# Performance work log

Hardware: AMD Instinct MI355X
Metric: run time of the kernel (lower is better)

The kernel has to match this reference:

```python
import jax, jax.numpy as jnp
import numpy as np

N_NODES = 50000

def cheb_conv(x, edge_index, W, b):
    # PyG ChebConv, K=2, normalization='sym', lambda_max=2.0 (default):
    # scaled Laplacian L_hat = (2/lambda_max)*L - I = -D^{-1/2} A D^{-1/2} (zero diag).
    # Tx_0 = x, Tx_1 = L_hat @ x ; out = Tx_0 @ W[0] + Tx_1 @ W[1] + b
    src, dst = edge_index[0], edge_index[1]
    ones = jnp.ones(src.shape[0], x.dtype)
    deg = jax.ops.segment_sum(ones, src, num_segments=N_NODES)
    dinv = jnp.where(deg > 0, 1.0 / jnp.sqrt(deg), 0.0)
    norm = -dinv[src] * dinv[dst]                                   # [E]
    tx1 = jax.ops.segment_sum(x[src] * norm[:, None], dst, num_segments=N_NODES)
    return x @ W[0] + tx1 @ W[1] + b

def setup_inputs() -> dict:
    key = jax.random.key(0)
    ks = jax.random.split(key, 12)
    IN, OUT, E, P = 128, 2, 800000, 400000
    return {
        "x": jax.random.normal(ks[0], (N_NODES, IN), jnp.float32),
        "edge_index": jax.random.randint(ks[1], (2, E), 0, N_NODES),
        "E_pos": jax.random.randint(ks[2], (2, P), 0, N_NODES),
        "neg_edge_index": jax.random.randint(ks[3], (2, P), 0, N_NODES),
        "W1": jax.random.normal(ks[4], (2, IN, 300), jnp.float32) * 0.05,
        "b1": jnp.zeros((300,), jnp.float32),
        "W2": jax.random.normal(ks[5], (2, 300, 100), jnp.float32) * 0.05,
        "b2": jnp.zeros((100,), jnp.float32),
        "W3": jax.random.normal(ks[6], (2, 100, OUT), jnp.float32) * 0.05,
        "b3": jnp.zeros((OUT,), jnp.float32),
        "lin1_W": jax.random.normal(ks[7], (100, IN), jnp.float32) * 0.05,
        "lin1_b": jnp.zeros((100,), jnp.float32),
        "lin2_W": jax.random.normal(ks[8], (100, IN), jnp.float32) * 0.05,
        "lin2_b": jnp.zeros((100,), jnp.float32),
        "c1": jnp.full((1,), 0.5, jnp.float32),
        "c2": jnp.full((1,), 0.5, jnp.float32),
    }

def reference(x, edge_index, E_pos, neg_edge_index, W1, b1, W2, b2, W3, b3,
              lin1_W, lin1_b, lin2_W, lin2_b, c1, c2):
    # eval mode: F.dropout and dropout_edge are identity
    x0 = x
    h = jax.nn.relu(cheb_conv(x0, edge_index, W1, b1))
    x1 = jax.nn.relu(cheb_conv(h, edge_index, W2, b2))
    x2 = x1 + jax.nn.relu(x0 @ lin1_W.T + lin1_b)
    z = x1 + jax.nn.relu(x0 @ lin2_W.T + lin2_b)
    pos_score = jnp.sum(z[E_pos[0]] * z[E_pos[1]], axis=1)              # [P]
    pos_loss = -jnp.mean(jnp.log(jax.nn.sigmoid(pos_score) + 1e-15))
    neg_score = jnp.sum(z[neg_edge_index[0]] * z[neg_edge_index[1]], axis=1)
    neg_loss = -jnp.mean(jnp.log(1.0 - jax.nn.sigmoid(neg_score) + 1e-15))
    r_loss = pos_loss + neg_loss
    out = cheb_conv(x2, edge_index, W3, b3)                             # [N, out_channels]
    return (out, r_loss, c1, c2)
```

## Files before the change

### kernel.cpp

```cpp
#include <hip/hip_runtime.h>
#include <math.h>


typedef unsigned short ushort_t;
typedef unsigned char u8;
typedef __attribute__((ext_vector_type(8))) __bf16 bf16x8;
typedef __attribute__((ext_vector_type(8))) short s16x8;
typedef __attribute__((ext_vector_type(4))) float f32x4;
typedef __attribute__((ext_vector_type(2))) float f32x2;

__device__ __forceinline__ f32x4 mfma16x16x32(s16x8 a, s16x8 b, f32x4 c) {
  return __builtin_amdgcn_mfma_f32_16x16x32_bf16(
      __builtin_bit_cast(bf16x8, a), __builtin_bit_cast(bf16x8, b), c, 0, 0, 0);
}
__device__ __forceinline__ ushort_t f2bf(float f) {
  union { float f; unsigned u; } c; c.f = f;
  unsigned r = (c.u + 0x7FFFu + ((c.u >> 16) & 1u)) >> 16;
  return (ushort_t)r;
}
__device__ __forceinline__ float blo(unsigned u) {
  union { unsigned u; float f; } c; c.u = u << 16; return c.f;
}
__device__ __forceinline__ float bhi(unsigned u) {
  union { unsigned u; float f; } c; c.u = u & 0xffff0000u; return c.f;
}
__device__ __forceinline__ f32x2 cvt2lo(unsigned u) {
  return __builtin_amdgcn_cvt_pk_f32_fp8((int)u, false);
}
__device__ __forceinline__ f32x2 cvt2hi(unsigned u) {
  return __builtin_amdgcn_cvt_pk_f32_fp8((int)u, true);
}
__device__ __forceinline__ u8 f2fp8(float f) {
  return (u8)(__builtin_amdgcn_cvt_pk_fp8_f32(f, 0.f, 0, false) & 0xff);
}

template<int VAR, int NT, int KTOT>
__global__ __launch_bounds__(256) void gemm_mfma(
    const ushort_t* __restrict__ A0, const ushort_t* __restrict__ A1,
    const ushort_t* __restrict__ Wt,
    const float* __restrict__ bias0, const float* __restrict__ bias1,
    const float* __restrict__ x1,
    const float* __restrict__ W3c, const float* __restrict__ b3c,
    void* __restrict__ out0, void* __restrict__ out1,
    float* __restrict__ t0g, float* __restrict__ t1g, int M)
{
  constexpr int NF = NT / 32;
  __shared__ __align__(16) ushort_t As[64 * 40];
  __shared__ __align__(16) ushort_t Bs[NT * 40];
  __shared__ float w3s[400];
  const int tid  = threadIdx.x;
  const int lane = tid & 63, w = tid >> 6;
  const int m0 = blockIdx.x * 64;
  const int wm = (w & 1) * 32, wn = (w >> 1) * (NT / 2);
  if (VAR == 2) { for (int i = tid; i < 400; i += 256) w3s[i] = W3c[i]; }
  f32x4 acc[2][NF];
#pragma unroll
  for (int i = 0; i < 2; ++i)
#pragma unroll
    for (int j = 0; j < NF; ++j) acc[i][j] = (f32x4){0.f, 0.f, 0.f, 0.f};

  for (int k0 = 0; k0 < KTOT; k0 += 32) {
    {
      const int r = tid >> 2, c8 = (tid & 3) * 8;
      const int gm = m0 + r;
      uint4 v = {0u, 0u, 0u, 0u};
      if (gm < M) {
        const ushort_t* srcp;
        if (VAR == 0) srcp = (k0 < 128) ? A0 + (size_t)gm * 128 + k0 + c8
                                        : A1 + (size_t)gm * 128 + (k0 - 128) + c8;
        else if (VAR == 1) srcp = A0 + (size_t)gm * 320 + k0 + c8;
        else srcp = A0 + (size_t)gm * 128 + k0 + c8;
        v = *(const uint4*)srcp;
      }
      *(uint4*)&As[r * 40 + c8] = v;
    }
    {
      const int c8 = (tid & 3) * 8;
#pragma unroll
      for (int i = 0; i < (NT * 4 + 255) / 256; ++i) {
        const int r = (tid >> 2) + i * 64;
        if (r < NT)
          *(uint4*)&Bs[r * 40 + c8] = *(const uint4*)(Wt + (size_t)r * KTOT + k0 + c8);
      }
    }
    __syncthreads();
    s16x8 af[2], bfr[NF];
#pragma unroll
    for (int mi = 0; mi < 2; ++mi)
      af[mi] = *(const s16x8*)&As[(wm + mi * 16 + (lane & 15)) * 40 + (lane >> 4) * 8];
#pragma unroll
    for (int ni = 0; ni < NF; ++ni)
      bfr[ni] = *(const s16x8*)&Bs[(wn + ni * 16 + (lane & 15)) * 40 + (lane >> 4) * 8];
#pragma unroll
    for (int mi = 0; mi < 2; ++mi)
#pragma unroll
      for (int ni = 0; ni < NF; ++ni)
        acc[mi][ni] = mfma16x16x32(af[mi], bfr[ni], acc[mi][ni]);
    __syncthreads();
  }

  if (VAR == 2) {
#pragma unroll
    for (int mi = 0; mi < 2; ++mi)
#pragma unroll
      for (int r = 0; r < 4; ++r) {
        const int gRow = m0 + wm + mi * 16 + ((lane >> 4) << 2) + r;
        float p0 = 0.f, p1 = 0.f, p2 = 0.f, p3 = 0.f;
#pragma unroll
        for (int ni = 0; ni < NF; ++ni) {
          const int col = wn + ni * 16 + (lane & 15);
          const float v = acc[mi][ni][r];
          if (gRow < M) {
            if (col < 100) {
              const float x2v = x1[(size_t)gRow * 128 + col] + fmaxf(v + bias0[col], 0.f);
              p0 = fmaf(x2v, w3s[col * 2 + 0], p0);
              p1 = fmaf(x2v, w3s[col * 2 + 1], p1);
              p2 = fmaf(x2v, w3s[200 + col * 2 + 0], p2);
              p3 = fmaf(x2v, w3s[200 + col * 2 + 1], p3);
            } else if (col < 200) {
              const int c = col - 100;
              ((u8*)out1)[(size_t)gRow * 128 + c] =
                  f2fp8(x1[(size_t)gRow * 128 + c] + fmaxf(v + bias1[c], 0.f));
            }
          }
        }
        if (wn == 0) {
#pragma unroll
          for (int off = 8; off; off >>= 1) {
            p0 += __shfl_down(p0, off, 16);
            p1 += __shfl_down(p1, off, 16);
            p2 += __shfl_down(p2, off, 16);
            p3 += __shfl_down(p3, off, 16);
          }
          if ((lane & 15) == 0 && gRow < M) {
            t0g[(size_t)gRow * 2 + 0] = p0 + b3c[0];
            t0g[(size_t)gRow * 2 + 1] = p1 + b3c[1];
            t1g[(size_t)gRow * 2 + 0] = p2;
            t1g[(size_t)gRow * 2 + 1] = p3;
          }
        }
      }
  } else {
#pragma unroll
    for (int mi = 0; mi < 2; ++mi)
#pragma unroll
      for (int ni = 0; ni < NF; ++ni)
#pragma unroll
        for (int r = 0; r < 4; ++r) {
          const int gRow = m0 + wm + mi * 16 + ((lane >> 4) << 2) + r;
          const int col  = wn + ni * 16 + (lane & 15);
          if (gRow >= M) continue;
          const float v = acc[mi][ni][r];
          if (VAR == 0) {
            ushort_t* h = (ushort_t*)out0;
            h[(size_t)gRow * 320 + col] = (col < 300) ? f2bf(fmaxf(v + bias0[col], 0.f))
                                                      : (ushort_t)0;
          } else {
            if (col < 100) ((float*)out0)[(size_t)gRow * 128 + col] = v + bias0[col];
            else if (col < 200) ((u8*)out1)[(size_t)gRow * 128 + (col - 100)] = f2fp8(v);
          }
        }
  }
}

__global__ void cvt_x_kernel(const float* __restrict__ x, ushort_t* __restrict__ xb,
                             u8* __restrict__ xf8, int n4) {
  const int i = blockIdx.x * 256 + threadIdx.x;
  if (i < n4) {
    const float4 v = ((const float4*)x)[i];
    ushort4 o; o.x = f2bf(v.x); o.y = f2bf(v.y); o.z = f2bf(v.z); o.w = f2bf(v.w);
    ((ushort4*)xb)[i] = o;
    int p = 0;
    p = __builtin_amdgcn_cvt_pk_fp8_f32(v.x, v.y, p, false);
    p = __builtin_amdgcn_cvt_pk_fp8_f32(v.z, v.w, p, true);
    ((unsigned*)xf8)[i] = (unsigned)p;
  }
}
__global__ void pack_all(const float* __restrict__ W1, const float* __restrict__ W2,
                         const float* __restrict__ l1W, const float* __restrict__ l2W,
                         ushort_t* __restrict__ W1t, ushort_t* __restrict__ W2t,
                         ushort_t* __restrict__ Wlt) {
  const int i = blockIdx.x * 256 + threadIdx.x;
  if (i < 81920) {
    const int n = i >> 8, k = i & 255;
    float v = 0.f;
    if (n < 300) v = (k < 128) ? W1[k * 300 + n] : W1[38400 + (k - 128) * 300 + n];
    W1t[i] = f2bf(v);
  } else if (i < 153600) {
    const int j = i - 81920;
    const int n = j / 320, k = j - n * 320;
    float v = 0.f;
    if (n < 200 && k < 300) v = W2[(n < 100 ? 0 : 30000) + k * 100 + (n % 100)];
    W2t[j] = f2bf(v);
  } else if (i < 182272) {
    const int j = i - 153600;
    const int n = j >> 7, k = j & 127;
    float v = 0.f;
    if (n < 100) v = l1W[n * 128 + k];
    else if (n < 200) v = l2W[(n - 100) * 128 + k];
    Wlt[j] = f2bf(v);
  }
}

__global__ void deg_count_kernel(const int* __restrict__ src, const int* __restrict__ dst,
                                 float* __restrict__ deg, int* __restrict__ cnt, int E)
{
  const int e = blockIdx.x * blockDim.x + threadIdx.x;
  if (e < E) { atomicAdd(deg + src[e], 1.0f); atomicAdd(cnt + dst[e], 1); }
}
__global__ void dinv_kernel(float* __restrict__ d, int n) {
  const int i = blockIdx.x * blockDim.x + threadIdx.x;
  if (i < n) { const float v = d[i]; d[i] = (v > 0.f) ? 1.f / sqrtf(v) : 0.f; }
}

__global__ void scan_local(const int* __restrict__ cnt, int* __restrict__ ptr,
                           int* __restrict__ bsum, int n)
{
  __shared__ int tmp[256];
  const int i = blockIdx.x * 256 + threadIdx.x;
  const int v = (i < n) ? cnt[i] : 0;
  tmp[threadIdx.x] = v;
  __syncthreads();
  for (int off = 1; off < 256; off <<= 1) {
    const int t = (threadIdx.x >= off) ? tmp[threadIdx.x - off] : 0;
    __syncthreads();
    tmp[threadIdx.x] += t;
    __syncthreads();
  }
  if (i < n) ptr[i] = tmp[threadIdx.x] - v;
  if (threadIdx.x == 255) bsum[blockIdx.x] = tmp[255];
}
__global__ void scan_bsum(int* __restrict__ bsum, int nb) {
  __shared__ int tmp[256];
  const int v = (threadIdx.x < nb) ? bsum[threadIdx.x] : 0;
  tmp[threadIdx.x] = v;
  __syncthreads();
  for (int off = 1; off < 256; off <<= 1) {
    const int t = (threadIdx.x >= off) ? tmp[threadIdx.x - off] : 0;
    __syncthreads();
    tmp[threadIdx.x] += t;
    __syncthreads();
  }
  if (threadIdx.x < nb) bsum[threadIdx.x] = tmp[threadIdx.x] - v;
}
__global__ void scan_add(int* __restrict__ ptr, const int* __restrict__ bsum, int n, int E) {
  const int i = blockIdx.x * 256 + threadIdx.x;
  if (i < n) ptr[i] += bsum[blockIdx.x];
  if (i == 0) ptr[n] = E;
}
__global__ void fill_csr(const int* __restrict__ src, const int* __restrict__ dst,
                         const float* __restrict__ dinv, int* __restrict__ cur,
                         int* __restrict__ cs, float* __restrict__ cw, int E)
{
  const int e = blockIdx.x * blockDim.x + threadIdx.x;
  if (e >= E) return;
  const int s = src[e], d = dst[e];
  const int pos = atomicAdd(cur + d, 1);
  cs[pos] = s;
  cw[pos] = -dinv[s] * dinv[d];
}

#define ACCV(u, ww) { f32x2 t; \
  t = cvt2lo(u.x); a[0]  = fmaf(ww, t.x, a[0]);  a[1]  = fmaf(ww, t.y, a[1]);  \
  t = cvt2hi(u.x); a[2]  = fmaf(ww, t.x, a[2]);  a[3]  = fmaf(ww, t.y, a[3]);  \
  t = cvt2lo(u.y); a[4]  = fmaf(ww, t.x, a[4]);  a[5]  = fmaf(ww, t.y, a[5]);  \
  t = cvt2hi(u.y); a[6]  = fmaf(ww, t.x, a[6]);  a[7]  = fmaf(ww, t.y, a[7]);  \
  t = cvt2lo(u.z); a[8]  = fmaf(ww, t.x, a[8]);  a[9]  = fmaf(ww, t.y, a[9]);  \
  t = cvt2hi(u.z); a[10] = fmaf(ww, t.x, a[10]); a[11] = fmaf(ww, t.y, a[11]); \
  t = cvt2lo(u.w); a[12] = fmaf(ww, t.x, a[12]); a[13] = fmaf(ww, t.y, a[13]); \
  t = cvt2hi(u.w); a[14] = fmaf(ww, t.x, a[14]); a[15] = fmaf(ww, t.y, a[15]); }

__global__ __launch_bounds__(256) void gather128e(
    const u8* __restrict__ xf8, ushort_t* __restrict__ txb,
    const int* __restrict__ ptr, const int* __restrict__ cs,
    const float* __restrict__ cw, int M)
{
  const int node = (blockIdx.x * 256 + threadIdx.x) >> 3;
  const int sub  = threadIdx.x & 7;
  if (node >= M) return;
  const int beg = ptr[node], end = ptr[node + 1];
  float a[16] = {};
  int p = beg;
  for (; p + 4 <= end; p += 4) {
    const int s0 = cs[p], s1 = cs[p + 1], s2 = cs[p + 2], s3 = cs[p + 3];
    const float w0 = cw[p], w1 = cw[p + 1], w2 = cw[p + 2], w3 = cw[p + 3];
    const uint4 v0 = *(const uint4*)(xf8 + (size_t)s0 * 128 + sub * 16);
    const uint4 v1 = *(const uint4*)(xf8 + (size_t)s1 * 128 + sub * 16);
    const uint4 v2 = *(const uint4*)(xf8 + (size_t)s2 * 128 + sub * 16);
    const uint4 v3 = *(const uint4*)(xf8 + (size_t)s3 * 128 + sub * 16);
    ACCV(v0, w0) ACCV(v1, w1) ACCV(v2, w2) ACCV(v3, w3)
  }
  for (; p < end; ++p) {
    const int s = cs[p]; const float wq = cw[p];
    const uint4 v = *(const uint4*)(xf8 + (size_t)s * 128 + sub * 16);
    ACCV(v, wq)
  }
  uint4 o1, o2;
  o1.x = (unsigned)f2bf(a[0])  | ((unsigned)f2bf(a[1])  << 16);
  o1.y = (unsigned)f2bf(a[2])  | ((unsigned)f2bf(a[3])  << 16);
  o1.z = (unsigned)f2bf(a[4])  | ((unsigned)f2bf(a[5])  << 16);
  o1.w = (unsigned)f2bf(a[6])  | ((unsigned)f2bf(a[7])  << 16);
  o2.x = (unsigned)f2bf(a[8])  | ((unsigned)f2bf(a[9])  << 16);
  o2.y = (unsigned)f2bf(a[10]) | ((unsigned)f2bf(a[11]) << 16);
  o2.z = (unsigned)f2bf(a[12]) | ((unsigned)f2bf(a[13]) << 16);
  o2.w = (unsigned)f2bf(a[14]) | ((unsigned)f2bf(a[15]) << 16);
  ushort_t* dstp = txb + (size_t)node * 128 + sub * 16;
  *(uint4*)dstp = o1;
  *(uint4*)(dstp + 8) = o2;
}

__global__ __launch_bounds__(256) void gather100e_x1(
    const u8* __restrict__ Brh, float* __restrict__ Ar,
    const int* __restrict__ ptr, const int* __restrict__ cs,
    const float* __restrict__ cw, int M)
{
  const int node = (blockIdx.x * 256 + threadIdx.x) >> 3;
  const int sub  = threadIdx.x & 7;
  if (node >= M) return;
  const int beg = ptr[node], end = ptr[node + 1];
  float a[16] = {};
  int p = beg;
  for (; p + 4 <= end; p += 4) {
    const int s0 = cs[p], s1 = cs[p + 1], s2 = cs[p + 2], s3 = cs[p + 3];
    const float w0 = cw[p], w1 = cw[p + 1], w2 = cw[p + 2], w3 = cw[p + 3];
    const uint4 v0 = *(const uint4*)(Brh + (size_t)s0 * 128 + sub * 16);
    const uint4 v1 = *(const uint4*)(Brh + (size_t)s1 * 128 + sub * 16);
    const uint4 v2 = *(const uint4*)(Brh + (size_t)s2 * 128 + sub * 16);
    const uint4 v3 = *(const uint4*)(Brh + (size_t)s3 * 128 + sub * 16);
    ACCV(v0, w0) ACCV(v1, w1) ACCV(v2, w2) ACCV(v3, w3)
  }
  for (; p < end; ++p) {
    const int s = cs[p]; const float wq = cw[p];
    const uint4 v = *(const uint4*)(Brh + (size_t)s * 128 + sub * 16);
    ACCV(v, wq)
  }
  float* dstp = Ar + (size_t)node * 128 + sub * 16;
#pragma unroll
  for (int q = 0; q < 4; ++q) {
    float4 b = *(const float4*)(dstp + q * 4);
    b.x = fmaxf(b.x + a[q * 4 + 0], 0.f);
    b.y = fmaxf(b.y + a[q * 4 + 1], 0.f);
    b.z = fmaxf(b.z + a[q * 4 + 2], 0.f);
    b.w = fmaxf(b.w + a[q * 4 + 3], 0.f);
    *(float4*)(dstp + q * 4) = b;
  }
}
#undef ACCV

#define DOTV(uu, vv, s) { f32x2 p_, q_; \
  p_ = cvt2lo(uu.x); q_ = cvt2lo(vv.x); s = fmaf(p_.x, q_.x, s); s = fmaf(p_.y, q_.y, s); \
  p_ = cvt2hi(uu.x); q_ = cvt2hi(vv.x); s = fmaf(p_.x, q_.x, s); s = fmaf(p_.y, q_.y, s); \
  p_ = cvt2lo(uu.y); q_ = cvt2lo(vv.y); s = fmaf(p_.x, q_.x, s); s = fmaf(p_.y, q_.y, s); \
  p_ = cvt2hi(uu.y); q_ = cvt2hi(vv.y); s = fmaf(p_.x, q_.x, s); s = fmaf(p_.y, q_.y, s); \
  p_ = cvt2lo(uu.z); q_ = cvt2lo(vv.z); s = fmaf(p_.x, q_.x, s); s = fmaf(p_.y, q_.y, s); \
  p_ = cvt2hi(uu.z); q_ = cvt2hi(vv.z); s = fmaf(p_.x, q_.x, s); s = fmaf(p_.y, q_.y, s); \
  p_ = cvt2lo(uu.w); q_ = cvt2lo(vv.w); s = fmaf(p_.x, q_.x, s); s = fmaf(p_.y, q_.y, s); \
  p_ = cvt2hi(uu.w); q_ = cvt2hi(vv.w); s = fmaf(p_.x, q_.x, s); s = fmaf(p_.y, q_.y, s); }

__global__ __launch_bounds__(256) void loss_fp8(
    const u8* __restrict__ zf8, const int* __restrict__ ep,
    const int* __restrict__ en, int P, float* __restrict__ acc)
{
  __shared__ float red[8];
  const int tid = threadIdx.x;
  const int lane = tid & 63, wib = tid >> 6;
  const int sub = tid & 7;
  const int slot0 = blockIdx.x * 32 + (tid >> 3);
  const int step = gridDim.x * 32;
  float tp = 0.f, tn = 0.f;
  int g = slot0;
  for (; g + step < 2 * P; g += 2 * step) {
    const int gA = g, gB = g + step;
    const int negA = (gA >= P), negB = (gB >= P);
    const int pA = negA ? gA - P : gA, pB = negB ? gB - P : gB;
    const int* iA = negA ? en : ep;
    const int* iB = negB ? en : ep;
    const int naA = iA[pA], nbA = iA[P + pA];
    const int naB = iB[pB], nbB = iB[P + pB];
    const uint4 ra1 = *(const uint4*)(zf8 + (size_t)naA * 128 + sub * 16);
    const uint4 rb1 = *(const uint4*)(zf8 + (size_t)nbA * 128 + sub * 16);
    const uint4 ra2 = *(const uint4*)(zf8 + (size_t)naB * 128 + sub * 16);
    const uint4 rb2 = *(const uint4*)(zf8 + (size_t)nbB * 128 + sub * 16);
    float sA = 0.f, sB = 0.f;
    DOTV(ra1, rb1, sA)
    DOTV(ra2, rb2, sB)
#pragma unroll
    for (int off = 4; off; off >>= 1) {
      sA += __shfl_down(sA, off, 8);
      sB += __shfl_down(sB, off, 8);
    }
    if (sub == 0) {
      const float gA_ = 1.f / (1.f + expf(-sA));
      if (negA) tn += logf(1.f - gA_ + 1e-15f); else tp += logf(gA_ + 1e-15f);
      const float gB_ = 1.f / (1.f + expf(-sB));
      if (negB) tn += logf(1.f - gB_ + 1e-15f); else tp += logf(gB_ + 1e-15f);
    }
  }
  if (g < 2 * P) {
    const int neg = (g >= P);
    const int p = neg ? g - P : g;
    const int* ia = neg ? en : ep;
    const int na = ia[p], nb = ia[P + p];
    const uint4 ra = *(const uint4*)(zf8 + (size_t)na * 128 + sub * 16);
    const uint4 rb = *(const uint4*)(zf8 + (size_t)nb * 128 + sub * 16);
    float s = 0.f;
    DOTV(ra, rb, s)
#pragma unroll
    for (int off = 4; off; off >>= 1) s += __shfl_down(s, off, 8);
    if (sub == 0) {
      const float sig = 1.f / (1.f + expf(-s));
      if (neg) tn += logf(1.f - sig + 1e-15f); else tp += logf(sig + 1e-15f);
    }
  }
  tp += __shfl_down(tp, 32, 64); tn += __shfl_down(tn, 32, 64);
  tp += __shfl_down(tp, 16, 64); tn += __shfl_down(tn, 16, 64);
  tp += __shfl_down(tp, 8, 64);  tn += __shfl_down(tn, 8, 64);
  if (lane == 0) { red[wib] = tp; red[4 + wib] = tn; }
  __syncthreads();
  if (tid == 0) {
    atomicAdd(acc + 0, red[0] + red[1] + red[2] + red[3]);
    atomicAdd(acc + 1, red[4] + red[5] + red[6] + red[7]);
  }
}
#undef DOTV

__global__ void gather2_final(
    const float* __restrict__ t1, const float* __restrict__ t0,
    const int* __restrict__ ptr, const int* __restrict__ cs,
    const float* __restrict__ cw, const float* __restrict__ accs,
    const float* __restrict__ c1, const float* __restrict__ c2,
    float* __restrict__ out, int M, float invP)
{
  const int i = blockIdx.x * blockDim.x + threadIdx.x;
  if (i < M) {
    float a0 = 0.f, a1 = 0.f;
    const int beg = ptr[i], end = ptr[i + 1];
    int p = beg;
    for (; p + 4 <= end; p += 4) {
      const int s0 = cs[p], s1 = cs[p + 1], s2 = cs[p + 2], s3 = cs[p + 3];
      const float w0 = cw[p], w1 = cw[p + 1], w2 = cw[p + 2], w3 = cw[p + 3];
      const float2 v0 = *(const float2*)(t1 + (size_t)s0 * 2);
      const float2 v1 = *(const float2*)(t1 + (size_t)s1 * 2);
      const float2 v2 = *(const float2*)(t1 + (size_t)s2 * 2);
      const float2 v3 = *(const float2*)(t1 + (size_t)s3 * 2);
      a0 = fmaf(w0, v0.x, a0); a1 = fmaf(w0, v0.y, a1);
      a0 = fmaf(w1, v1.x, a0); a1 = fmaf(w1, v1.y, a1);
      a0 = fmaf(w2, v2.x, a0); a1 = fmaf(w2, v2.y, a1);
      a0 = fmaf(w3, v3.x, a0); a1 = fmaf(w3, v3.y, a1);
    }
    for (; p < end; ++p) {
      const int s = cs[p]; const float w = cw[p];
      const float2 v = *(const float2*)(t1 + (size_t)s * 2);
      a0 = fmaf(w, v.x, a0); a1 = fmaf(w, v.y, a1);
    }
    const float2 base = *(const float2*)(t0 + (size_t)i * 2);
    *(float2*)(out + (size_t)i * 2) = make_float2(base.x + a0, base.y + a1);
  }
  if (i == 0) {
    out[2 * M + 0] = -(accs[0] + accs[1]) * invP;
    out[2 * M + 1] = c1[0];
    out[2 * M + 2] = c2[0];
  }
}

extern "C" void kernel_launch(void* const* d_in, const int* in_sizes, int n_in,
                              void* d_out, int out_size, void* d_ws, size_t ws_size,
                              hipStream_t stream)
{
  const float* x   = (const float*)d_in[0];
  const int*   ei  = (const int*)d_in[1];
  const int*   ep  = (const int*)d_in[2];
  const int*   en  = (const int*)d_in[3];
  const float* W1  = (const float*)d_in[4];
  const float* b1  = (const float*)d_in[5];
  const float* W2  = (const float*)d_in[6];
  const float* b2  = (const float*)d_in[7];
  const float* W3  = (const float*)d_in[8];
  const float* b3  = (const float*)d_in[9];
  const float* l1W = (const float*)d_in[10];
  const float* l1b = (const float*)d_in[11];
  const float* l2W = (const float*)d_in[12];
  const float* l2b = (const float*)d_in[13];
  const float* c1  = (const float*)d_in[14];
  const float* c2  = (const float*)d_in[15];
  float* out = (float*)d_out;

  const int M = in_sizes[0] / 128;
  const int E = in_sizes[1] / 2;
  const int P = in_sizes[2] / 2;
  const int* src = ei;
  const int* dst = ei + E;
  const int nb_scan = (M + 255) / 256;

  float* ws = (float*)d_ws;
  size_t o = 0;
  float*    dinv = ws + o;            o += 50176;
  int*      cnt  = (int*)(ws + o);    o += (size_t)M;
  int*      ptr  = (int*)(ws + o);    o += (size_t)M + 8;
  int*      cur  = (int*)(ws + o);    o += (size_t)M;
  int*      bsum = (int*)(ws + o);    o += 256;
  int*      csr_s = (int*)(ws + o);   o += (size_t)E;
  float*    csr_w = ws + o;           o += (size_t)E;
  ushort_t* xb   = (ushort_t*)(ws + o); o += (size_t)M * 64;
  u8*       xf8  = (u8*)(ws + o);     o += (size_t)M * 32;
  ushort_t* tx0b = (ushort_t*)(ws + o); o += (size_t)M * 64;
  ushort_t* W1t  = (ushort_t*)(ws + o); o += 40960;
  ushort_t* W2t  = (ushort_t*)(ws + o); o += 35840;
  ushort_t* Wlt  = (ushort_t*)(ws + o); o += 14336;
  ushort_t* h    = (ushort_t*)(ws + o); o += (size_t)M * 160;
  float*    Ar   = ws + o;            o += (size_t)M * 128;
  u8*       Brh  = (u8*)(ws + o);     o += (size_t)M * 32;
  u8*       zf8  = (u8*)(ws + o);     o += (size_t)M * 32;
  float*    t0   = ws + o;            o += (size_t)M * 2;
  float*    t1   = ws + o;            o += (size_t)M * 2;
  float*    accs = ws + o;            o += 8;

  hipMemsetAsync(dinv, 0, (size_t)M * 4, stream);
  hipMemsetAsync(cnt,  0, (size_t)M * 4, stream);
  hipMemsetAsync(accs, 0, 2 * 4, stream);
  hipMemsetAsync(Brh,  0, (size_t)M * 128, stream);
  hipMemsetAsync(zf8,  0, (size_t)M * 128, stream);

  cvt_x_kernel<<<(M * 32 + 255) / 256, 256, 0, stream>>>(x, xb, xf8, M * 32);
  pack_all<<<(182272 + 255) / 256, 256, 0, stream>>>(W1, W2, l1W, l2W, W1t, W2t, Wlt);

  deg_count_kernel<<<(E + 255) / 256, 256, 0, stream>>>(src, dst, dinv, cnt, E);
  dinv_kernel<<<(M + 255) / 256, 256, 0, stream>>>(dinv, M);
  scan_local<<<nb_scan, 256, 0, stream>>>(cnt, ptr, bsum, M);
  scan_bsum<<<1, 256, 0, stream>>>(bsum, nb_scan);
  scan_add<<<nb_scan, 256, 0, stream>>>(ptr, bsum, M, E);
  hipMemcpyAsync(cur, ptr, (size_t)M * 4, hipMemcpyDeviceToDevice, stream);
  fill_csr<<<(E + 255) / 256, 256, 0, stream>>>(src, dst, dinv, cur, csr_s, csr_w, E);

  const int gB = (M + 63) / 64;
  const int gE8 = (M * 8 + 255) / 256;

  gather128e<<<gE8, 256, 0, stream>>>(xf8, tx0b, ptr, csr_s, csr_w, M);
  gemm_mfma<0, 320, 256><<<gB, 256, 0, stream>>>(
      xb, tx0b, W1t, b1, nullptr, nullptr, nullptr, nullptr, h, nullptr, nullptr, nullptr, M);

  gemm_mfma<1, 224, 320><<<gB, 256, 0, stream>>>(
      h, nullptr, W2t, b2, nullptr, nullptr, nullptr, nullptr, Ar, Brh, nullptr, nullptr, M);
  gather100e_x1<<<gE8, 256, 0, stream>>>(Brh, Ar, ptr, csr_s, csr_w, M);

  gemm_mfma<2, 224, 128><<<gB, 256, 0, stream>>>(
      xb, nullptr, Wlt, l1b, l2b, Ar , W3, b3, nullptr, zf8, t0, t1, M);

  loss_fp8<<<2048, 256, 0, stream>>>(zf8, ep, en, P, accs);

  gather2_final<<<(M + 255) / 256, 256, 0, stream>>>(t1, t0, ptr, csr_s, csr_w,
                                                     accs, c1, c2, out, M, 1.0f / (float)P);
}
```

Baseline: 532.9 us.

## Build CSR via per-block shared-memory histograms and ranks instead of global atomics

Replaces the global-atomic degree count and atomic-cursor CSR fill with a two-pass scheme. 64 blocks build range-partitioned shared-memory histograms of src and dst and record each edge's rank within its block. Per-block counts are then reduced and prefix-summed so each edge's slot can be computed without atomics, which also makes the CSR order deterministic. The source index and weight are packed into one int2 array so the gathers issue one load per edge. In exchange, each edge is reread eight times across histogram rounds, only 64 blocks are launched, and extra partial tables of size 64×M are written and read.

```diff
diff --git a/kernel.cpp b/kernel.cpp
--- a/kernel.cpp
+++ b/kernel.cpp
@@ -9,6 +9,10 @@
 typedef __attribute__((ext_vector_type(4))) float f32x4;
 typedef __attribute__((ext_vector_type(2))) float f32x2;
 
+#define NB_H 64
+#define NR 4
+#define RK 12800
+
 __device__ __forceinline__ f32x4 mfma16x16x32(s16x8 a, s16x8 b, f32x4 c) {
   return __builtin_amdgcn_mfma_f32_16x16x32_bf16(
       __builtin_bit_cast(bf16x8, a), __builtin_bit_cast(bf16x8, b), c, 0, 0, 0);
@@ -17,12 +21,6 @@
   union { float f; unsigned u; } c; c.f = f;
   unsigned r = (c.u + 0x7FFFu + ((c.u >> 16) & 1u)) >> 16;
   return (ushort_t)r;
-}
-__device__ __forceinline__ float blo(unsigned u) {
-  union { unsigned u; float f; } c; c.u = u << 16; return c.f;
-}
-__device__ __forceinline__ float bhi(unsigned u) {
-  union { unsigned u; float f; } c; c.u = u & 0xffff0000u; return c.f;
 }
 __device__ __forceinline__ f32x2 cvt2lo(unsigned u) {
   return __builtin_amdgcn_cvt_pk_f32_fp8((int)u, false);
@@ -202,15 +200,65 @@
   }
 }
 
-__global__ void deg_count_kernel(const int* __restrict__ src, const int* __restrict__ dst,
-                                 float* __restrict__ deg, int* __restrict__ cnt, int E)
-{
-  const int e = blockIdx.x * blockDim.x + threadIdx.x;
-  if (e < E) { atomicAdd(deg + src[e], 1.0f); atomicAdd(cnt + dst[e], 1); }
-}
-__global__ void dinv_kernel(float* __restrict__ d, int n) {
-  const int i = blockIdx.x * blockDim.x + threadIdx.x;
-  if (i < n) { const float v = d[i]; d[i] = (v > 0.f) ? 1.f / sqrtf(v) : 0.f; }
+__global__ __launch_bounds__(256) void hist_rank(
+    const int* __restrict__ src, const int* __restrict__ dst, int E, int M,
+    ushort_t* __restrict__ partS, ushort_t* __restrict__ partD,
+    ushort_t* __restrict__ rank)
+{
+  __shared__ unsigned hist[RK];
+  const int b = blockIdx.x;
+  const int cs = (E + NB_H - 1) / NB_H;
+  const int e0 = b * cs;
+  const int e1 = (e0 + cs < E) ? e0 + cs : E;
+  for (int isD = 0; isD < 2; ++isD) {
+    const int* keys = isD ? dst : src;
+    ushort_t* part = isD ? partD : partS;
+    for (int r = 0; r < NR; ++r) {
+      const int klo = r * RK;
+      for (int i = threadIdx.x; i < RK; i += 256) hist[i] = 0;
+      __syncthreads();
+      for (int e = e0 + threadIdx.x; e < e1; e += 256) {
+        const int k = keys[e] - klo;
+        if ((unsigned)k < (unsigned)RK) {
+          const unsigned old = atomicAdd(&hist[k], 1u);
+          if (isD) rank[e] = (ushort_t)old;
+        }
+      }
+      __syncthreads();
+      for (int i = threadIdx.x; i < RK; i += 256) {
+        const int k = klo + i;
+        if (k < M) part[(size_t)b * M + k] = (ushort_t)hist[i];
+      }
+      __syncthreads();
+    }
+  }
+}
+
+__global__ void reduce_hist(const ushort_t* __restrict__ partS,
+                            const ushort_t* __restrict__ partD,
+                            float* __restrict__ dinv, int* __restrict__ cnt, int M)
+{
+  const int k = blockIdx.x * 256 + threadIdx.x;
+  if (k >= M) return;
+  unsigned s = 0, d = 0;
+  for (int b = 0; b < NB_H; ++b) {
+    s += partS[(size_t)b * M + k];
+    d += partD[(size_t)b * M + k];
+  }
+  dinv[k] = (s > 0) ? 1.f / sqrtf((float)s) : 0.f;
+  cnt[k] = (int)d;
+}
+
+__global__ void base_tab(const ushort_t* __restrict__ partD,
+                         ushort_t* __restrict__ base16, int M)
+{
+  const int k = blockIdx.x * 256 + threadIdx.x;
+  if (k >= M) return;
+  unsigned run = 0;
+  for (int b = 0; b < NB_H; ++b) {
+    base16[(size_t)b * M + k] = (ushort_t)run;
+    run += partD[(size_t)b * M + k];
+  }
 }
 
 __global__ void scan_local(const int* __restrict__ cnt, int* __restrict__ ptr,
@@ -248,16 +296,20 @@
   if (i < n) ptr[i] += bsum[blockIdx.x];
   if (i == 0) ptr[n] = E;
 }
-__global__ void fill_csr(const int* __restrict__ src, const int* __restrict__ dst,
-                         const float* __restrict__ dinv, int* __restrict__ cur,
-                         int* __restrict__ cs, float* __restrict__ cw, int E)
-{
-  const int e = blockIdx.x * blockDim.x + threadIdx.x;
+__global__ void fill_csr2(const int* __restrict__ src, const int* __restrict__ dst,
+                          const float* __restrict__ dinv, const int* __restrict__ ptr,
+                          const ushort_t* __restrict__ base16,
+                          const ushort_t* __restrict__ rank,
+                          int2* __restrict__ csr, int E, int M)
+{
+  const int e = blockIdx.x * 256 + threadIdx.x;
   if (e >= E) return;
+  const int cs = (E + NB_H - 1) / NB_H;
+  const int b = e / cs;
   const int s = src[e], d = dst[e];
-  const int pos = atomicAdd(cur + d, 1);
-  cs[pos] = s;
-  cw[pos] = -dinv[s] * dinv[d];
+  const int pos = ptr[d] + (int)base16[(size_t)b * M + d] + (int)rank[e];
+  const float w = -dinv[s] * dinv[d];
+  csr[pos] = make_int2(s, __float_as_int(w));
 }
 
 #define ACCV(u, ww) { f32x2 t; \
@@ -272,8 +324,7 @@
 
 __global__ __launch_bounds__(256) void gather128e(
     const u8* __restrict__ xf8, ushort_t* __restrict__ txb,
-    const int* __restrict__ ptr, const int* __restrict__ cs,
-    const float* __restrict__ cw, int M)
+    const int* __restrict__ ptr, const int2* __restrict__ csr, int M)
 {
   const int node = (blockIdx.x * 256 + threadIdx.x) >> 3;
   const int sub  = threadIdx.x & 7;
@@ -282,17 +333,18 @@
   float a[16] = {};
   int p = beg;
   for (; p + 4 <= end; p += 4) {
-    const int s0 = cs[p], s1 = cs[p + 1], s2 = cs[p + 2], s3 = cs[p + 3];
-    const float w0 = cw[p], w1 = cw[p + 1], w2 = cw[p + 2], w3 = cw[p + 3];
-    const uint4 v0 = *(const uint4*)(xf8 + (size_t)s0 * 128 + sub * 16);
-    const uint4 v1 = *(const uint4*)(xf8 + (size_t)s1 * 128 + sub * 16);
-    const uint4 v2 = *(const uint4*)(xf8 + (size_t)s2 * 128 + sub * 16);
-    const uint4 v3 = *(const uint4*)(xf8 + (size_t)s3 * 128 + sub * 16);
+    const int2 e0 = csr[p], e1 = csr[p + 1], e2 = csr[p + 2], e3 = csr[p + 3];
+    const float w0 = __int_as_float(e0.y), w1 = __int_as_float(e1.y);
+    const float w2 = __int_as_float(e2.y), w3 = __int_as_float(e3.y);
+    const uint4 v0 = *(const uint4*)(xf8 + (size_t)e0.x * 128 + sub * 16);
+    const uint4 v1 = *(const uint4*)(xf8 + (size_t)e1.x * 128 + sub * 16);
+    const uint4 v2 = *(const uint4*)(xf8 + (size_t)e2.x * 128 + sub * 16);
+    const uint4 v3 = *(const uint4*)(xf8 + (size_t)e3.x * 128 + sub * 16);
     ACCV(v0, w0) ACCV(v1, w1) ACCV(v2, w2) ACCV(v3, w3)
   }
   for (; p < end; ++p) {
-    const int s = cs[p]; const float wq = cw[p];
-    const uint4 v = *(const uint4*)(xf8 + (size_t)s * 128 + sub * 16);
+    const int2 eq = csr[p]; const float wq = __int_as_float(eq.y);
+    const uint4 v = *(const uint4*)(xf8 + (size_t)eq.x * 128 + sub * 16);
     ACCV(v, wq)
   }
   uint4 o1, o2;
@@ -311,8 +363,7 @@
 
 __global__ __launch_bounds__(256) void gather100e_x1(
     const u8* __restrict__ Brh, float* __restrict__ Ar,
-    const int* __restrict__ ptr, const int* __restrict__ cs,
-    const float* __restrict__ cw, int M)
+    const int* __restrict__ ptr, const int2* __restrict__ csr, int M)
 {
   const int node = (blockIdx.x * 256 + threadIdx.x) >> 3;
   const int sub  = threadIdx.x & 7;
@@ -321,17 +372,18 @@
   float a[16] = {};
   int p = beg;
   for (; p + 4 <= end; p += 4) {
-    const int s0 = cs[p], s1 = cs[p + 1], s2 = cs[p + 2], s3 = cs[p + 3];
-    const float w0 = cw[p], w1 = cw[p + 1], w2 = cw[p + 2], w3 = cw[p + 3];
-    const uint4 v0 = *(const uint4*)(Brh + (size_t)s0 * 128 + sub * 16);
-    const uint4 v1 = *(const uint4*)(Brh + (size_t)s1 * 128 + sub * 16);
-    const uint4 v2 = *(const uint4*)(Brh + (size_t)s2 * 128 + sub * 16);
-    const uint4 v3 = *(const uint4*)(Brh + (size_t)s3 * 128 + sub * 16);
+    const int2 e0 = csr[p], e1 = csr[p + 1], e2 = csr[p + 2], e3 = csr[p + 3];
+    const float w0 = __int_as_float(e0.y), w1 = __int_as_float(e1.y);
+    const float w2 = __int_as_float(e2.y), w3 = __int_as_float(e3.y);
+    const uint4 v0 = *(const uint4*)(Brh + (size_t)e0.x * 128 + sub * 16);
+    const uint4 v1 = *(const uint4*)(Brh + (size_t)e1.x * 128 + sub * 16);
+    const uint4 v2 = *(const uint4*)(Brh + (size_t)e2.x * 128 + sub * 16);
+    const uint4 v3 = *(const uint4*)(Brh + (size_t)e3.x * 128 + sub * 16);
     ACCV(v0, w0) ACCV(v1, w1) ACCV(v2, w2) ACCV(v3, w3)
   }
   for (; p < end; ++p) {
-    const int s = cs[p]; const float wq = cw[p];
-    const uint4 v = *(const uint4*)(Brh + (size_t)s * 128 + sub * 16);
+    const int2 eq = csr[p]; const float wq = __int_as_float(eq.y);
+    const uint4 v = *(const uint4*)(Brh + (size_t)eq.x * 128 + sub * 16);
     ACCV(v, wq)
   }
   float* dstp = Ar + (size_t)node * 128 + sub * 16;
@@ -426,8 +478,8 @@
 
 __global__ void gather2_final(
     const float* __restrict__ t1, const float* __restrict__ t0,
-    const int* __restrict__ ptr, const int* __restrict__ cs,
-    const float* __restrict__ cw, const float* __restrict__ accs,
+    const int* __restrict__ ptr, const int2* __restrict__ csr,
+    const float* __restrict__ accs,
     const float* __restrict__ c1, const float* __restrict__ c2,
     float* __restrict__ out, int M, float invP)
 {
@@ -437,21 +489,22 @@
     const int beg = ptr[i], end = ptr[i + 1];
     int p = beg;
     for (; p + 4 <= end; p += 4) {
-      const int s0 = cs[p], s1 = cs[p + 1], s2 = cs[p + 2], s3 = cs[p + 3];
-      const float w0 = cw[p], w1 = cw[p + 1], w2 = cw[p + 2], w3 = cw[p + 3];
-      const float2 v0 = *(const float2*)(t1 + (size_t)s0 * 2);
-      const float2 v1 = *(const float2*)(t1 + (size_t)s1 * 2);
-      const float2 v2 = *(const float2*)(t1 + (size_t)s2 * 2);
-      const float2 v3 = *(const float2*)(t1 + (size_t)s3 * 2);
+      const int2 e0 = csr[p], e1 = csr[p + 1], e2 = csr[p + 2], e3 = csr[p + 3];
+      const float w0 = __int_as_float(e0.y), w1 = __int_as_float(e1.y);
+      const float w2 = __int_as_float(e2.y), w3 = __int_as_float(e3.y);
+      const float2 v0 = *(const float2*)(t1 + (size_t)e0.x * 2);
+      const float2 v1 = *(const float2*)(t1 + (size_t)e1.x * 2);
+      const float2 v2 = *(const float2*)(t1 + (size_t)e2.x * 2);
+      const float2 v3 = *(const float2*)(t1 + (size_t)e3.x * 2);
       a0 = fmaf(w0, v0.x, a0); a1 = fmaf(w0, v0.y, a1);
       a0 = fmaf(w1, v1.x, a0); a1 = fmaf(w1, v1.y, a1);
       a0 = fmaf(w2, v2.x, a0); a1 = fmaf(w2, v2.y, a1);
       a0 = fmaf(w3, v3.x, a0); a1 = fmaf(w3, v3.y, a1);
     }
     for (; p < end; ++p) {
-      const int s = cs[p]; const float w = cw[p];
-      const float2 v = *(const float2*)(t1 + (size_t)s * 2);
-      a0 = fmaf(w, v.x, a0); a1 = fmaf(w, v.y, a1);
+      const int2 eq = csr[p]; const float wq = __int_as_float(eq.y);
+      const float2 v = *(const float2*)(t1 + (size_t)eq.x * 2);
+      a0 = fmaf(wq, v.x, a0); a1 = fmaf(wq, v.y, a1);
     }
     const float2 base = *(const float2*)(t0 + (size_t)i * 2);
     *(float2*)(out + (size_t)i * 2) = make_float2(base.x + a0, base.y + a1);
@@ -497,10 +550,11 @@
   float*    dinv = ws + o;            o += 50176;
   int*      cnt  = (int*)(ws + o);    o += (size_t)M;
   int*      ptr  = (int*)(ws + o);    o += (size_t)M + 8;
-  int*      cur  = (int*)(ws + o);    o += (size_t)M;
   int*      bsum = (int*)(ws + o);    o += 256;
-  int*      csr_s = (int*)(ws + o);   o += (size_t)E;
-  float*    csr_w = ws + o;           o += (size_t)E;
+  int2*     csr  = (int2*)(ws + o);   o += (size_t)E * 2;
+  ushort_t* partS = (ushort_t*)(ws + o); o += (size_t)NB_H * M / 2;
+  ushort_t* partD = (ushort_t*)(ws + o); o += (size_t)NB_H * M / 2;
+  ushort_t* rank  = (ushort_t*)(ws + o); o += (size_t)E / 2;
   ushort_t* xb   = (ushort_t*)(ws + o); o += (size_t)M * 64;
   u8*       xf8  = (u8*)(ws + o);     o += (size_t)M * 32;
   ushort_t* tx0b = (ushort_t*)(ws + o); o += (size_t)M * 64;
@@ -514,9 +568,8 @@
   float*    t0   = ws + o;            o += (size_t)M * 2;
   float*    t1   = ws + o;            o += (size_t)M * 2;
   float*    accs = ws + o;            o += 8;
-
-  hipMemsetAsync(dinv, 0, (size_t)M * 4, stream);
-  hipMemsetAsync(cnt,  0, (size_t)M * 4, stream);
+  ushort_t* base16 = partS;
+
   hipMemsetAsync(accs, 0, 2 * 4, stream);
   hipMemsetAsync(Brh,  0, (size_t)M * 128, stream);
   hipMemsetAsync(zf8,  0, (size_t)M * 128, stream);
@@ -524,30 +577,30 @@
   cvt_x_kernel<<<(M * 32 + 255) / 256, 256, 0, stream>>>(x, xb, xf8, M * 32);
   pack_all<<<(182272 + 255) / 256, 256, 0, stream>>>(W1, W2, l1W, l2W, W1t, W2t, Wlt);
 
-  deg_count_kernel<<<(E + 255) / 256, 256, 0, stream>>>(src, dst, dinv, cnt, E);
-  dinv_kernel<<<(M + 255) / 256, 256, 0, stream>>>(dinv, M);
+  hist_rank<<<NB_H, 256, 0, stream>>>(src, dst, E, M, partS, partD, rank);
+  reduce_hist<<<(M + 255) / 256, 256, 0, stream>>>(partS, partD, dinv, cnt, M);
   scan_local<<<nb_scan, 256, 0, stream>>>(cnt, ptr, bsum, M);
   scan_bsum<<<1, 256, 0, stream>>>(bsum, nb_scan);
   scan_add<<<nb_scan, 256, 0, stream>>>(ptr, bsum, M, E);
-  hipMemcpyAsync(cur, ptr, (size_t)M * 4, hipMemcpyDeviceToDevice, stream);
-  fill_csr<<<(E + 255) / 256, 256, 0, stream>>>(src, dst, dinv, cur, csr_s, csr_w, E);
+  base_tab<<<(M + 255) / 256, 256, 0, stream>>>(partD, base16, M);
+  fill_csr2<<<(E + 255) / 256, 256, 0, stream>>>(src, dst, dinv, ptr, base16, rank, csr, E, M);
 
   const int gB = (M + 63) / 64;
   const int gE8 = (M * 8 + 255) / 256;
 
-  gather128e<<<gE8, 256, 0, stream>>>(xf8, tx0b, ptr, csr_s, csr_w, M);
+  gather128e<<<gE8, 256, 0, stream>>>(xf8, tx0b, ptr, csr, M);
   gemm_mfma<0, 320, 256><<<gB, 256, 0, stream>>>(
       xb, tx0b, W1t, b1, nullptr, nullptr, nullptr, nullptr, h, nullptr, nullptr, nullptr, M);
 
   gemm_mfma<1, 224, 320><<<gB, 256, 0, stream>>>(
       h, nullptr, W2t, b2, nullptr, nullptr, nullptr, nullptr, Ar, Brh, nullptr, nullptr, M);
-  gather100e_x1<<<gE8, 256, 0, stream>>>(Brh, Ar, ptr, csr_s, csr_w, M);
+  gather100e_x1<<<gE8, 256, 0, stream>>>(Brh, Ar, ptr, csr, M);
 
   gemm_mfma<2, 224, 128><<<gB, 256, 0, stream>>>(
       xb, nullptr, Wlt, l1b, l2b, Ar , W3, b3, nullptr, zf8, t0, t1, M);
 
   loss_fp8<<<2048, 256, 0, stream>>>(zf8, ep, en, P, accs);
 
-  gather2_final<<<(M + 255) / 256, 256, 0, stream>>>(t1, t0, ptr, csr_s, csr_w,
+  gather2_final<<<(M + 255) / 256, 256, 0, stream>>>(t1, t0, ptr, csr,
                                                      accs, c1, c2, out, M, 1.0f / (float)P);
 }
```

After: 567.8 us. +6.5%, slower.
